# Optimization experiments

Measured on AMD Instinct MI355X. Metric: run time of the kernel, lower is better.

The kernel has to match this reference:

```python
import jax, jax.numpy as jnp
import numpy as np

N, E = 50000, 800000
DIN, H, DOUT, L = 128, 128, 64, 3
NEG_SLOPE = 0.2  # PyG GATConv default


def setup_inputs() -> dict:
    key = jax.random.key(0)
    ks = jax.random.split(key, 12)
    s = lambda i, shape: (jax.random.normal(ks[i], shape, jnp.float32) * 0.05)
    return {
        "x": jax.random.normal(ks[0], (N, DIN), jnp.float32),
        "edge_index": jax.random.randint(ks[1], (2, E), 0, N, jnp.int64 if jax.config.jax_enable_x64 else jnp.int32),
        "W_emb": s(2, (DIN, H)), "b_emb": jnp.zeros((H,), jnp.float32),
        "gat_W": s(3, (L, H, H)), "gat_as": s(4, (L, H)), "gat_ad": s(5, (L, H)),
        "gat_b": jnp.zeros((L, H), jnp.float32),
        "Wn1": s(6, (H, H)), "bn1": jnp.zeros((H,), jnp.float32),
        "Wn2": s(7, (H, DOUT)), "bn2": jnp.zeros((DOUT,), jnp.float32),
        "We1": s(8, (2 * H, H)), "be1": jnp.zeros((H,), jnp.float32),
        "We2": s(9, (H, 3)), "be2": jnp.zeros((3,), jnp.float32),
    }


def _gat_layer(h, src, dst, n, W, a_src, a_dst, b):
    # Single-head GATConv (PyG defaults: heads=1, concat, self-loops already in src/dst)
    xw = h @ W                                   # [N, H]
    alpha_s = xw @ a_src                          # [N]
    alpha_d = xw @ a_dst                          # [N]
    logits = jax.nn.leaky_relu(alpha_s[src] + alpha_d[dst], NEG_SLOPE)  # [E']
    m = jax.ops.segment_max(logits, dst, num_segments=n)
    p = jnp.exp(logits - m[dst])
    denom = jax.ops.segment_sum(p, dst, num_segments=n)
    alpha = p / denom[dst]                        # softmax over incoming edges
    return jax.ops.segment_sum(alpha[:, None] * xw[src], dst, num_segments=n) + b


def reference(x, edge_index, W_emb, b_emb, gat_W, gat_as, gat_ad, gat_b,
              Wn1, bn1, Wn2, bn2, We1, be1, We2, be2):
    n = x.shape[0]
    src0, dst0 = edge_index[0], edge_index[1]
    loops = jnp.arange(n, dtype=src0.dtype)
    src = jnp.concatenate([src0, loops])          # GATConv adds self-loops by default
    dst = jnp.concatenate([dst0, loops])

    h = jax.nn.relu(x @ W_emb + b_emb)            # dropout off (eval mode)
    for l in range(L):
        h_new = _gat_layer(h, src, dst, n, gat_W[l], gat_as[l], gat_ad[l], gat_b[l])
        h = jax.nn.relu(h + h_new)                # residual + relu

    node_pred = jax.nn.relu(h @ Wn1 + bn1) @ Wn2 + bn2            # [N, DOUT]
    ef = jnp.concatenate([h[src0], h[dst0]], axis=1)              # vectorized edge gather [E, 2H]
    edge_pred = jax.nn.relu(ef @ We1 + be1) @ We2 + be2           # [E, 3]
    graph_emb = jnp.mean(h, axis=0, keepdims=True)                # batch=None path [1, H]
    return node_pred, edge_pred, graph_emb
```

## Files before the change

kernel.cpp:

```cpp
#include <hip/hip_runtime.h>

#define NNODES 50000
#define NEDGES 800000
#define HDIM 128
#define DOUT 64
#define NLAYERS 3
#define NEG_SLOPE 0.2f

#define NODE_OUT_ELEMS (NNODES * DOUT)
#define EDGE_OUT_ELEMS (NEDGES * 3)
#define GEMB_OFF (NODE_OUT_ELEMS + EDGE_OUT_ELEMS)

typedef __attribute__((ext_vector_type(8))) short short8;
typedef __attribute__((ext_vector_type(4))) float f32x4;

__device__ __forceinline__ float bf2f(unsigned short u) {
    union { unsigned int i; float f; } v; v.i = ((unsigned int)u) << 16; return v.f;
}
__device__ __forceinline__ unsigned short f2bf(float f) {
    union { unsigned int i; float f; } v; v.f = f;
    unsigned int b = v.i;
    unsigned int r = (b + 0x7FFFu + ((b >> 16) & 1u)) >> 16;
    return (unsigned short)r;
}
__device__ __forceinline__ float leaky(float x) { return x > 0.f ? x : NEG_SLOPE * x; }

__device__ __forceinline__ int eget(const int* e32, const int* iflag, int which, int e) {
    int idx = which * NEDGES + e;
    return (*iflag) ? e32[idx] : e32[2 * idx];
}

__global__ void zero_int_kernel(int* p, int n) {
    int i = blockIdx.x * 256 + threadIdx.x;
    if (i < n) p[i] = 0;
}
__global__ void zero_f32_kernel(float* p, int n) {
    int i = blockIdx.x * 256 + threadIdx.x;
    if (i < n) p[i] = 0.f;
}

__global__ void detect_f32_kernel(const unsigned short* xb, int* flag) {
    int hit = 0;
    for (int j = threadIdx.x; j < 4096; j += 256) {
        int e = (xb[j] >> 7) & 0xFF;
        if (e >= 0x90) hit = 1;
    }
    if (hit) atomicOr(flag, 1);
}
__global__ void detect_i64_kernel(const int* e32, int* flag) {
    int hit = 0;
    for (int t = threadIdx.x; t < 16384; t += 256) {
        int i = t * 48;
        if (e32[2 * i + 1] != 0) hit = 1;
    }
    if (__any(hit)) {
        if ((threadIdx.x & 63) == 0) atomicOr(flag, 1);
    }
}

__global__ void cvt_kernel(const void* src, float* dst, int n, const int* f32flag) {
    int i = blockIdx.x * 256 + threadIdx.x;
    if (i < n)
        dst[i] = (*f32flag) ? ((const float*)src)[i]
                            : bf2f(((const unsigned short*)src)[i]);
}
__global__ void cvt_layerW_kernel(const void* gat_W, float* dst, int l,
                                  const int* f32flag) {
    int i = blockIdx.x * 256 + threadIdx.x;
    if (i < HDIM * HDIM) {
        size_t idx = (size_t)l * HDIM * HDIM + i;
        dst[i] = (*f32flag) ? ((const float*)gat_W)[idx]
                            : bf2f(((const unsigned short*)gat_W)[idx]);
    }
}

struct SmallCvtArgs {
    const void* src[9];
    float*      dst[9];
    int         n[9];
};
__global__ void cvt_small_kernel(SmallCvtArgs a, const int* f32flag) {
    const int f = *f32flag;
    for (int s = 0; s < 9; s++) {
        int n = a.n[s];
        const void* sp = a.src[s];
        float* dp = a.dst[s];
        for (int i = blockIdx.x * 256 + threadIdx.x; i < n; i += gridDim.x * 256)
            dp[i] = f ? ((const float*)sp)[i]
                      : bf2f(((const unsigned short*)sp)[i]);
    }
}

__global__ void cvt_x_bf16_kernel(const void* x, unsigned short* xb,
                                  const int* f32flag) {
    int i = (blockIdx.x * 256 + threadIdx.x) * 4;
    if (*f32flag) {
        float4 v = *(const float4*)((const float*)x + i);
        unsigned short o[4] = {f2bf(v.x), f2bf(v.y), f2bf(v.z), f2bf(v.w)};
        *(uint2*)(xb + i) = *(uint2*)o;
    } else {
        *(uint2*)(xb + i) = *(const uint2*)((const unsigned short*)x + i);
    }
}

__global__ __launch_bounds__(256) void gemm_mfma_kernel(
    const unsigned short* __restrict__ A, const float* __restrict__ Bf,
    const float* __restrict__ bias, unsigned short* __restrict__ C,
    int M, int relu)
{
    constexpr int KP = 128 + 8;
    __shared__ unsigned short sA[64 * KP];
    const int tid = threadIdx.x;
    const int row0 = blockIdx.x * 64;

    for (int c = tid; c < 64 * 16; c += 256) {
        int r = c >> 4, cp = c & 15;
        int gr = row0 + r;
        uint4 v = {0u, 0u, 0u, 0u};
        if (gr < M) v = *(const uint4*)(A + (size_t)gr * 128 + cp * 8);
        *(uint4*)(&sA[r * KP + cp * 8]) = v;
    }
    __syncthreads();

    const int wave = tid >> 6, lane = tid & 63;
    const int quad = lane >> 4, l15 = lane & 15;
    const int ncol0 = wave * 32;

    short8 bw[4][2];
    #pragma unroll
    for (int kk = 0; kk < 4; kk++)
        #pragma unroll
        for (int nt = 0; nt < 2; nt++) {
            int n = ncol0 + nt * 16 + l15;
            short8 t;
            #pragma unroll
            for (int j = 0; j < 8; j++)
                t[j] = (short)f2bf(Bf[(size_t)(kk * 32 + quad * 8 + j) * 128 + n]);
            bw[kk][nt] = t;
        }

    float bv[2];
    #pragma unroll
    for (int nt = 0; nt < 2; nt++)
        bv[nt] = bias ? bias[ncol0 + nt * 16 + l15] : 0.f;

    f32x4 acc[4][2];
    #pragma unroll
    for (int mt = 0; mt < 4; mt++)
        #pragma unroll
        for (int nt = 0; nt < 2; nt++) {
            acc[mt][nt][0] = bv[nt]; acc[mt][nt][1] = bv[nt];
            acc[mt][nt][2] = bv[nt]; acc[mt][nt][3] = bv[nt];
        }

    #pragma unroll
    for (int kk = 0; kk < 4; kk++) {
        short8 a[4];
        #pragma unroll
        for (int mt = 0; mt < 4; mt++)
            a[mt] = *(const short8*)(&sA[(mt * 16 + l15) * KP + kk * 32 + quad * 8]);
        #pragma unroll
        for (int mt = 0; mt < 4; mt++)
            #pragma unroll
            for (int nt = 0; nt < 2; nt++)
                acc[mt][nt] = __builtin_amdgcn_mfma_f32_16x16x32_bf16(
                    a[mt], bw[kk][nt], acc[mt][nt], 0, 0, 0);
    }

    #pragma unroll
    for (int mt = 0; mt < 4; mt++)
        #pragma unroll
        for (int nt = 0; nt < 2; nt++)
            #pragma unroll
            for (int q = 0; q < 4; q++) {
                int row = row0 + mt * 16 + quad * 4 + q;
                if (row < M) {
                    float v = acc[mt][nt][q];
                    if (relu) v = fmaxf(v, 0.f);
                    C[(size_t)row * 128 + ncol0 + nt * 16 + l15] = f2bf(v);
                }
            }
}

__global__ __launch_bounds__(256) void node_mlp_kernel(
    const unsigned short* __restrict__ h, const float* __restrict__ Wn1f,
    const float* __restrict__ bn1, const float* __restrict__ Wn2f,
    const float* __restrict__ bn2, float* __restrict__ out, int M)
{
    constexpr int KP = 128 + 8;
    __shared__ unsigned short sA[64 * KP];
    const int tid = threadIdx.x;
    const int row0 = blockIdx.x * 64;

    for (int c = tid; c < 64 * 16; c += 256) {
        int r = c >> 4, cp = c & 15;
        int gr = row0 + r;
        uint4 v = {0u, 0u, 0u, 0u};
        if (gr < M) v = *(const uint4*)(h + (size_t)gr * 128 + cp * 8);
        *(uint4*)(&sA[r * KP + cp * 8]) = v;
    }
    __syncthreads();

    const int wave = tid >> 6, lane = tid & 63;
    const int quad = lane >> 4, l15 = lane & 15;
    const int ncol0 = wave * 32;

    {
        short8 bw[4][2];
        #pragma unroll
        for (int kk = 0; kk < 4; kk++)
            #pragma unroll
            for (int nt = 0; nt < 2; nt++) {
                int n = ncol0 + nt * 16 + l15;
                short8 t;
                #pragma unroll
                for (int j = 0; j < 8; j++)
                    t[j] = (short)f2bf(Wn1f[(size_t)(kk * 32 + quad * 8 + j) * 128 + n]);
                bw[kk][nt] = t;
            }
        float bv[2];
        #pragma unroll
        for (int nt = 0; nt < 2; nt++) bv[nt] = bn1[ncol0 + nt * 16 + l15];

        f32x4 acc[4][2];
        #pragma unroll
        for (int mt = 0; mt < 4; mt++)
            #pragma unroll
            for (int nt = 0; nt < 2; nt++) {
                acc[mt][nt][0] = bv[nt]; acc[mt][nt][1] = bv[nt];
                acc[mt][nt][2] = bv[nt]; acc[mt][nt][3] = bv[nt];
            }
        #pragma unroll
        for (int kk = 0; kk < 4; kk++) {
            short8 a[4];
            #pragma unroll
            for (int mt = 0; mt < 4; mt++)
                a[mt] = *(const short8*)(&sA[(mt * 16 + l15) * KP + kk * 32 + quad * 8]);
            #pragma unroll
            for (int mt = 0; mt < 4; mt++)
                #pragma unroll
                for (int nt = 0; nt < 2; nt++)
                    acc[mt][nt] = __builtin_amdgcn_mfma_f32_16x16x32_bf16(
                        a[mt], bw[kk][nt], acc[mt][nt], 0, 0, 0);
        }
        __syncthreads();
        #pragma unroll
        for (int mt = 0; mt < 4; mt++)
            #pragma unroll
            for (int nt = 0; nt < 2; nt++)
                #pragma unroll
                for (int q = 0; q < 4; q++) {
                    int r = mt * 16 + quad * 4 + q;
                    sA[r * KP + ncol0 + nt * 16 + l15] =
                        f2bf(fmaxf(acc[mt][nt][q], 0.f));
                }
        __syncthreads();
    }

    {
        const int col = wave * 16 + l15;
        short8 bw[4];
        #pragma unroll
        for (int kk = 0; kk < 4; kk++) {
            short8 t;
            #pragma unroll
            for (int j = 0; j < 8; j++)
                t[j] = (short)f2bf(Wn2f[(size_t)(kk * 32 + quad * 8 + j) * 64 + col]);
            bw[kk] = t;
        }
        float bv = bn2[col];
        f32x4 acc[4];
        #pragma unroll
        for (int mt = 0; mt < 4; mt++) {
            acc[mt][0] = bv; acc[mt][1] = bv; acc[mt][2] = bv; acc[mt][3] = bv;
        }
        #pragma unroll
        for (int kk = 0; kk < 4; kk++) {
            short8 a[4];
            #pragma unroll
            for (int mt = 0; mt < 4; mt++)
                a[mt] = *(const short8*)(&sA[(mt * 16 + l15) * KP + kk * 32 + quad * 8]);
            #pragma unroll
            for (int mt = 0; mt < 4; mt++)
                acc[mt] = __builtin_amdgcn_mfma_f32_16x16x32_bf16(
                    a[mt], bw[kk], acc[mt], 0, 0, 0);
        }
        #pragma unroll
        for (int mt = 0; mt < 4; mt++)
            #pragma unroll
            for (int q = 0; q < 4; q++) {
                int row = row0 + mt * 16 + quad * 4 + q;
                if (row < M) out[(size_t)row * 64 + col] = acc[mt][q];
            }
    }
}

__global__ __launch_bounds__(256) void edge_ab_kernel(
    const unsigned short* __restrict__ h, const float* __restrict__ We1f,
    const float* __restrict__ be1, unsigned short* __restrict__ Axw,
    unsigned short* __restrict__ Bh, int M)
{
    constexpr int KP = 128 + 8;
    __shared__ unsigned short sA[64 * KP];
    const int tid = threadIdx.x;
    const int row0 = blockIdx.x * 64;

    for (int c = tid; c < 64 * 16; c += 256) {
        int r = c >> 4, cp = c & 15;
        int gr = row0 + r;
        uint4 v = {0u, 0u, 0u, 0u};
        if (gr < M) v = *(const uint4*)(h + (size_t)gr * 128 + cp * 8);
        *(uint4*)(&sA[r * KP + cp * 8]) = v;
    }
    __syncthreads();

    const int wave = tid >> 6, lane = tid & 63;
    const int quad = lane >> 4, l15 = lane & 15;
    const int ncol0 = wave * 32;

    #pragma unroll
    for (int half = 0; half < 2; half++) {
        const float* Bf = We1f + (size_t)half * 128 * 128;
        unsigned short* Cp = half ? Bh : Axw;

        short8 bw[4][2];
        #pragma unroll
        for (int kk = 0; kk < 4; kk++)
            #pragma unroll
            for (int nt = 0; nt < 2; nt++) {
                int n = ncol0 + nt * 16 + l15;
                short8 t;
                #pragma unroll
                for (int j = 0; j < 8; j++)
                    t[j] = (short)f2bf(Bf[(size_t)(kk * 32 + quad * 8 + j) * 128 + n]);
                bw[kk][nt] = t;
            }
        float bv[2];
        #pragma unroll
        for (int nt = 0; nt < 2; nt++)
            bv[nt] = half ? 0.f : be1[ncol0 + nt * 16 + l15];

        f32x4 acc[4][2];
        #pragma unroll
        for (int mt = 0; mt < 4; mt++)
            #pragma unroll
            for (int nt = 0; nt < 2; nt++) {
                acc[mt][nt][0] = bv[nt]; acc[mt][nt][1] = bv[nt];
                acc[mt][nt][2] = bv[nt]; acc[mt][nt][3] = bv[nt];
            }
        #pragma unroll
        for (int kk = 0; kk < 4; kk++) {
            short8 a[4];
            #pragma unroll
            for (int mt = 0; mt < 4; mt++)
                a[mt] = *(const short8*)(&sA[(mt * 16 + l15) * KP + kk * 32 + quad * 8]);
            #pragma unroll
            for (int mt = 0; mt < 4; mt++)
                #pragma unroll
                for (int nt = 0; nt < 2; nt++)
                    acc[mt][nt] = __builtin_amdgcn_mfma_f32_16x16x32_bf16(
                        a[mt], bw[kk][nt], acc[mt][nt], 0, 0, 0);
        }
        #pragma unroll
        for (int mt = 0; mt < 4; mt++)
            #pragma unroll
            for (int nt = 0; nt < 2; nt++)
                #pragma unroll
                for (int q = 0; q < 4; q++) {
                    int row = row0 + mt * 16 + quad * 4 + q;
                    if (row < M)
                        Cp[(size_t)row * 128 + ncol0 + nt * 16 + l15] =
                            f2bf(acc[mt][nt][q]);
                }
    }
}

__global__ void alpha_kernel(const unsigned short* xw,
                             const float* a_s, const float* a_d,
                             float* alpha_s, float* alpha_d) {
    int wave = threadIdx.x >> 6, lane = threadIdx.x & 63;
    int n = blockIdx.x * 4 + wave;
    if (n >= NNODES) return;
    float v0 = bf2f(xw[(size_t)n * HDIM + lane]);
    float v1 = bf2f(xw[(size_t)n * HDIM + 64 + lane]);
    float ds = v0 * a_s[lane] + v1 * a_s[64 + lane];
    float dd = v0 * a_d[lane] + v1 * a_d[64 + lane];
    for (int d = 32; d >= 1; d >>= 1) { ds += __shfl_xor(ds, d); dd += __shfl_xor(dd, d); }
    if (lane == 0) { alpha_s[n] = ds; alpha_d[n] = dd; }
}

__global__ void count_kernel(const int* e32, const int* iflag, int* cnt) {
    int e = blockIdx.x * 256 + threadIdx.x;
    if (e < NEDGES) atomicAdd(&cnt[eget(e32, iflag, 1, e)], 1);
}
__global__ void scan1_kernel(const int* cnt, int* off, int* bsum) {
    __shared__ int s[256];
    int t = threadIdx.x, i = blockIdx.x * 256 + t;
    int v = (i < NNODES) ? cnt[i] : 0;
    s[t] = v;
    __syncthreads();
    for (int d = 1; d < 256; d <<= 1) {
        int add = (t >= d) ? s[t - d] : 0;
        __syncthreads();
        s[t] += add;
        __syncthreads();
    }
    if (i < NNODES) off[i] = s[t] - v;
    if (t == 255) bsum[blockIdx.x] = s[255];
}
__global__ void scan2_kernel(int* bsum, int nblk) {
    if (threadIdx.x == 0 && blockIdx.x == 0) {
        int run = 0;
        for (int c = 0; c < nblk; c++) { int t = bsum[c]; bsum[c] = run; run += t; }
    }
}
__global__ void scan3_kernel(int* off, const int* bsum) {
    int i = blockIdx.x * 256 + threadIdx.x;
    if (i < NNODES) off[i] += bsum[blockIdx.x];
}
__global__ void fill_kernel(const int* e32, const int* iflag, const int* off,
                            int* cur, int* csr_src, int* csr_dst, int* csr_eid,
                            int use_csr) {
    int e = blockIdx.x * 256 + threadIdx.x;
    if (e < NEDGES) {
        int sidx = eget(e32, iflag, 0, e);
        int d = eget(e32, iflag, 1, e);
        int p = atomicAdd(&cur[d], 1);
        int pos = off[d] + p;
        csr_src[pos] = sidx;
        if (use_csr) {
            csr_dst[pos] = d;
            csr_eid[pos] = e;
        }
    }
}

__global__ void aggregate_kernel(const unsigned short* __restrict__ xw,
                                 const float* __restrict__ as_, const float* __restrict__ ad_,
                                 const int* __restrict__ off, const int* __restrict__ csr_src,
                                 const float* __restrict__ gat_b, unsigned short* __restrict__ h) {
    int wave = threadIdx.x >> 6, lane = threadIdx.x & 63;
    int n = blockIdx.x * 4 + wave;
    if (n >= NNODES) return;
    int o0 = off[n];
    int o1 = (n == NNODES - 1) ? NEDGES : off[n + 1];
    int deg = o1 - o0;
    float adn = ad_[n];
    float lself = leaky(as_[n] + adn);

    int deg64 = deg < 64 ? deg : 64;
    int idxv = 0; float av = 0.f;
    if (lane < deg64) { idxv = csr_src[o0 + lane]; av = as_[idxv]; }

    float m = lself;
    if (lane < deg64) m = fmaxf(m, leaky(av + adn));
    for (int i = 64 + lane; i < deg; i += 64) {
        int s = csr_src[o0 + i];
        m = fmaxf(m, leaky(as_[s] + adn));
    }
    #pragma unroll
    for (int d = 32; d >= 1; d >>= 1) m = fmaxf(m, __shfl_xor(m, d));

    const int slot = lane >> 4;
    const int l15  = lane & 15;
    float denom = 0.f;
    float acc[8];
    #pragma unroll
    for (int k = 0; k < 8; k++) acc[k] = 0.f;

    for (int t0 = 0; t0 < deg64; t0 += 4) {
        int i = t0 + slot;
        int sidx   = __shfl(idxv, i);
        float aval = __shfl(av, i);
        if (i < deg64) {
            float p = __expf(leaky(aval + adn) - m);
            denom += p;
            uint4 rv = *(const uint4*)(xw + (size_t)sidx * HDIM + l15 * 8);
            const unsigned short* rp = (const unsigned short*)&rv;
            #pragma unroll
            for (int k = 0; k < 8; k++) acc[k] += p * bf2f(rp[k]);
        }
    }
    for (int i = 64 + slot; i < deg; i += 4) {
        int s = csr_src[o0 + i];
        float p = __expf(leaky(as_[s] + adn) - m);
        denom += p;
        uint4 rv = *(const uint4*)(xw + (size_t)s * HDIM + l15 * 8);
        const unsigned short* rp = (const unsigned short*)&rv;
        #pragma unroll
        for (int k = 0; k < 8; k++) acc[k] += p * bf2f(rp[k]);
    }

    #pragma unroll
    for (int d = 16; d <= 32; d <<= 1) {
        denom += __shfl_xor(denom, d);
        #pragma unroll
        for (int k = 0; k < 8; k++) acc[k] += __shfl_xor(acc[k], d);
    }

    float ps = __expf(lself - m);
    denom += ps;
    uint4 sv = *(const uint4*)(xw + (size_t)n * HDIM + l15 * 8);
    const unsigned short* sp = (const unsigned short*)&sv;
    #pragma unroll
    for (int k = 0; k < 8; k++) acc[k] += ps * bf2f(sp[k]);

    if (slot == 0) {
        float inv = 1.f / denom;
        size_t base = (size_t)n * HDIM + l15 * 8;
        uint4 hv = *(const uint4*)(h + base);
        const unsigned short* hp = (const unsigned short*)&hv;
        unsigned short outv[8];
        #pragma unroll
        for (int k = 0; k < 8; k++) {
            float hx = bf2f(hp[k]);
            float bx = gat_b[l15 * 8 + k];
            outv[k] = f2bf(fmaxf(hx + acc[k] * inv + bx, 0.f));
        }
        *(uint4*)(h + base) = *(uint4*)outv;
    }
}

__global__ __launch_bounds__(256) void edge_split_kernel(
    const unsigned short* __restrict__ A, const unsigned short* __restrict__ B,
    const int* __restrict__ e32, const int* __restrict__ iflag,
    const int* __restrict__ csr_src, const int* __restrict__ csr_dst,
    const int* __restrict__ csr_eid, int use_csr,
    const float* __restrict__ We2, const float* __restrict__ be2,
    float* __restrict__ eout)
{
    const int lane = threadIdx.x & 63;
    const int slot = lane >> 4, l15 = lane & 15;

    float w2[8][3];
    #pragma unroll
    for (int j = 0; j < 8; j++)
        #pragma unroll
        for (int c = 0; c < 3; c++)
            w2[j][c] = We2[(l15 * 8 + j) * 3 + c];
    const float bo0 = be2[0], bo1 = be2[1], bo2 = be2[2];

    const int gw = (blockIdx.x * 256 + threadIdx.x) >> 6;
    const int stride = gridDim.x * 16;
    for (int e = gw * 4 + slot; e < NEDGES; e += stride) {
        int s, d, oe;
        if (use_csr) { s = csr_src[e]; d = csr_dst[e]; oe = csr_eid[e]; }
        else {
            s = eget(e32, iflag, 0, e);
            d = eget(e32, iflag, 1, e);
            oe = e;
        }
        uint4 avv = *(const uint4*)(A + (size_t)s * HDIM + l15 * 8);
        uint4 bvv = *(const uint4*)(B + (size_t)d * HDIM + l15 * 8);
        const unsigned short* ap = (const unsigned short*)&avv;
        const unsigned short* bp = (const unsigned short*)&bvv;
        float s0 = 0.f, s1 = 0.f, s2 = 0.f;
        #pragma unroll
        for (int j = 0; j < 8; j++) {
            float v = fmaxf(bf2f(ap[j]) + bf2f(bp[j]), 0.f);
            s0 += v * w2[j][0]; s1 += v * w2[j][1]; s2 += v * w2[j][2];
        }
        #pragma unroll
        for (int dd = 1; dd < 16; dd <<= 1) {
            s0 += __shfl_xor(s0, dd);
            s1 += __shfl_xor(s1, dd);
            s2 += __shfl_xor(s2, dd);
        }
        if (l15 == 0) {
            eout[(size_t)oe * 3 + 0] = s0 + bo0;
            eout[(size_t)oe * 3 + 1] = s1 + bo1;
            eout[(size_t)oe * 3 + 2] = s2 + bo2;
        }
    }
}

__global__ void gsum_kernel(const unsigned short* h, float* gsum) {
    int f = threadIdx.x;
    float local = 0.f;
    int n0 = blockIdx.x * 200;
    for (int j = 0; j < 200; j++) local += bf2f(h[(size_t)(n0 + j) * HDIM + f]);
    atomicAdd(&gsum[f], local);
}
__global__ void gout_kernel(const float* gsum, float* out) {
    int f = threadIdx.x;
    out[GEMB_OFF + f] = gsum[f] * (1.f / (float)NNODES);
}

extern "C" __attribute__((visibility("default")))
void kernel_launch(void* const* d_in, const int* in_sizes, int n_in,
                   void* d_out, int out_size, void* d_ws, size_t ws_size,
                   hipStream_t stream) {
    const void* x      = d_in[0];
    const int*  eidx   = (const int*)d_in[1];
    const void* W_emb  = d_in[2];
    const void* b_emb  = d_in[3];
    const void* gat_W  = d_in[4];
    const void* gat_as = d_in[5];
    const void* gat_ad = d_in[6];
    const void* gat_b  = d_in[7];
    const void* Wn1    = d_in[8];
    const void* bn1    = d_in[9];
    const void* Wn2    = d_in[10];
    const void* bn2    = d_in[11];
    const void* We1    = d_in[12];
    const void* be1    = d_in[13];
    const void* We2    = d_in[14];
    const void* be2    = d_in[15];
    float* out = (float*)d_out;

    char* ws = (char*)d_ws;
    unsigned short* h       = (unsigned short*)(ws);
    unsigned short* xw      = (unsigned short*)(ws + 12800000);
    float*          alpha_s = (float*)(ws + 25600000);
    float*          alpha_d = (float*)(ws + 25800000);
    int*            cnt     = (int*)(ws + 26000000);
    int*            off     = (int*)(ws + 26200000);
    int*            bsum    = (int*)(ws + 26400000);
    float*          gsum    = (float*)(ws + 26401024);
    int*            iflag   = (int*)(ws + 26401536);
    int*            fflag   = (int*)(ws + 26401540);
    float*          We1c    = (float*)(ws + 26402048);
    float*          We2c    = (float*)(ws + 26533120);
    float*          asc     = (float*)(ws + 26534656);
    float*          adc     = (float*)(ws + 26536192);
    float*          gbc     = (float*)(ws + 26537728);
    float*          bembc   = (float*)(ws + 26539264);
    float*          bn1c    = (float*)(ws + 26539776);
    float*          bn2c    = (float*)(ws + 26540288);
    float*          be1c    = (float*)(ws + 26540544);
    float*          be2c    = (float*)(ws + 26541056);
    float*          Wlc     = (float*)(ws + 26542080);
    int*            csr_src = (int*)(ws + 26608000);
    int*            csr_dst = (int*)(ws + 29808000);
    int*            csr_eid = (int*)(ws + 33008000);

    float* Wembc = (float*)(ws + 26200000);
    float* Wn1c = (float*)(ws + 26000000);
    float* Wn2c = (float*)(ws + 26065536);

    const int use_csr = (ws_size >= (size_t)36208000) ? 1 : 0;

    const int node_blks = (NNODES + 255) / 256;
    const int edge_blks = (NEDGES + 255) / 256;
    const int g64       = (NNODES + 63) / 64;

    zero_int_kernel<<<1, 256, 0, stream>>>(iflag, 2);
    zero_int_kernel<<<node_blks, 256, 0, stream>>>(cnt, NNODES);
    zero_f32_kernel<<<1, 256, 0, stream>>>(gsum, HDIM);

    detect_f32_kernel<<<1, 256, 0, stream>>>((const unsigned short*)x, fflag);
    detect_i64_kernel<<<1, 256, 0, stream>>>(eidx, iflag);

    SmallCvtArgs sc;
    sc.src[0] = We2;   sc.dst[0] = We2c;  sc.n[0] = 128 * 3;
    sc.src[1] = gat_as; sc.dst[1] = asc;  sc.n[1] = 3 * 128;
    sc.src[2] = gat_ad; sc.dst[2] = adc;  sc.n[2] = 3 * 128;
    sc.src[3] = gat_b;  sc.dst[3] = gbc;  sc.n[3] = 3 * 128;
    sc.src[4] = b_emb;  sc.dst[4] = bembc; sc.n[4] = 128;
    sc.src[5] = bn1;    sc.dst[5] = bn1c; sc.n[5] = 128;
    sc.src[6] = bn2;    sc.dst[6] = bn2c; sc.n[6] = 64;
    sc.src[7] = be1;    sc.dst[7] = be1c; sc.n[7] = 128;
    sc.src[8] = be2;    sc.dst[8] = be2c; sc.n[8] = 3;
    cvt_small_kernel<<<2, 256, 0, stream>>>(sc, fflag);

    cvt_kernel<<<128, 256, 0, stream>>>(We1, We1c, 256 * 128, fflag);
    cvt_kernel<<<64, 256, 0, stream>>>(W_emb, Wembc, 128 * 128, fflag);

    cvt_x_bf16_kernel<<<6250, 256, 0, stream>>>(x, xw, fflag);
    gemm_mfma_kernel<<<g64, 256, 0, stream>>>(
        xw, Wembc, bembc, h, NNODES, 1);

    count_kernel<<<edge_blks, 256, 0, stream>>>(eidx, iflag, cnt);
    scan1_kernel<<<node_blks, 256, 0, stream>>>(cnt, off, bsum);
    scan2_kernel<<<1, 64, 0, stream>>>(bsum, node_blks);
    scan3_kernel<<<node_blks, 256, 0, stream>>>(off, bsum);
    zero_int_kernel<<<node_blks, 256, 0, stream>>>(cnt, NNODES);
    fill_kernel<<<edge_blks, 256, 0, stream>>>(eidx, iflag, off, cnt,
                                               csr_src, csr_dst, csr_eid, use_csr);

    cvt_kernel<<<64, 256, 0, stream>>>(Wn1, Wn1c, 128 * 128, fflag);
    cvt_kernel<<<32, 256, 0, stream>>>(Wn2, Wn2c, 128 * 64, fflag);

    for (int l = 0; l < NLAYERS; l++) {
        cvt_layerW_kernel<<<64, 256, 0, stream>>>(gat_W, Wlc, l, fflag);
        gemm_mfma_kernel<<<g64, 256, 0, stream>>>(
            h, Wlc, (const float*)0, xw, NNODES, 0);
        alpha_kernel<<<(NNODES + 3) / 4, 256, 0, stream>>>(
            xw, asc + l * HDIM, adc + l * HDIM, alpha_s, alpha_d);
        aggregate_kernel<<<(NNODES + 3) / 4, 256, 0, stream>>>(
            xw, alpha_s, alpha_d, off, csr_src, gbc + l * HDIM, h);
    }

    node_mlp_kernel<<<g64, 256, 0, stream>>>(
        h, Wn1c, bn1c, Wn2c, bn2c, out, NNODES);

    gsum_kernel<<<NNODES / 200, 128, 0, stream>>>(h, gsum);
    gout_kernel<<<1, 128, 0, stream>>>(gsum, out);

    edge_ab_kernel<<<g64, 256, 0, stream>>>(
        h, We1c, be1c, xw, h, NNODES);
    edge_split_kernel<<<2048, 256, 0, stream>>>(
        xw, h, eidx, iflag, csr_src, csr_dst, csr_eid, use_csr,
        We2c, be2c, out + NODE_OUT_ELEMS);
}
```

Baseline: 547.2 us.

## Drop weight conversion kernels, read raw weights in place, pack CSR entries

Result: slower. 567.8 us (+3.8%).

```diff
diff --git a/kernel.cpp b/kernel.cpp
--- a/kernel.cpp
+++ b/kernel.cpp
@@ -13,6 +13,7 @@
 
 typedef __attribute__((ext_vector_type(8))) short short8;
 typedef __attribute__((ext_vector_type(4))) float f32x4;
+typedef unsigned long long u64;
 
 __device__ __forceinline__ float bf2f(unsigned short u) {
     union { unsigned int i; float f; } v; v.i = ((unsigned int)u) << 16; return v.f;
@@ -24,70 +25,42 @@
     return (unsigned short)r;
 }
 __device__ __forceinline__ float leaky(float x) { return x > 0.f ? x : NEG_SLOPE * x; }
+__device__ __forceinline__ float wread(const void* p, size_t i, int f32) {
+    return f32 ? ((const float*)p)[i] : bf2f(((const unsigned short*)p)[i]);
+}
 
 __device__ __forceinline__ int eget(const int* e32, const int* iflag, int which, int e) {
     int idx = which * NEDGES + e;
     return (*iflag) ? e32[idx] : e32[2 * idx];
 }
 
-__global__ void zero_int_kernel(int* p, int n) {
+__global__ void init_kernel(int* cnt, int* cur, float* gsum, int* flags) {
     int i = blockIdx.x * 256 + threadIdx.x;
-    if (i < n) p[i] = 0;
-}
-__global__ void zero_f32_kernel(float* p, int n) {
-    int i = blockIdx.x * 256 + threadIdx.x;
-    if (i < n) p[i] = 0.f;
-}
-
-__global__ void detect_f32_kernel(const unsigned short* xb, int* flag) {
-    int hit = 0;
-    for (int j = threadIdx.x; j < 4096; j += 256) {
-        int e = (xb[j] >> 7) & 0xFF;
-        if (e >= 0x90) hit = 1;
-    }
-    if (hit) atomicOr(flag, 1);
-}
-__global__ void detect_i64_kernel(const int* e32, int* flag) {
-    int hit = 0;
-    for (int t = threadIdx.x; t < 16384; t += 256) {
-        int i = t * 48;
-        if (e32[2 * i + 1] != 0) hit = 1;
-    }
-    if (__any(hit)) {
-        if ((threadIdx.x & 63) == 0) atomicOr(flag, 1);
-    }
-}
-
-__global__ void cvt_kernel(const void* src, float* dst, int n, const int* f32flag) {
-    int i = blockIdx.x * 256 + threadIdx.x;
-    if (i < n)
-        dst[i] = (*f32flag) ? ((const float*)src)[i]
-                            : bf2f(((const unsigned short*)src)[i]);
-}
-__global__ void cvt_layerW_kernel(const void* gat_W, float* dst, int l,
-                                  const int* f32flag) {
-    int i = blockIdx.x * 256 + threadIdx.x;
-    if (i < HDIM * HDIM) {
-        size_t idx = (size_t)l * HDIM * HDIM + i;
-        dst[i] = (*f32flag) ? ((const float*)gat_W)[idx]
-                            : bf2f(((const unsigned short*)gat_W)[idx]);
-    }
-}
-
-struct SmallCvtArgs {
-    const void* src[9];
-    float*      dst[9];
-    int         n[9];
-};
-__global__ void cvt_small_kernel(SmallCvtArgs a, const int* f32flag) {
-    const int f = *f32flag;
-    for (int s = 0; s < 9; s++) {
-        int n = a.n[s];
-        const void* sp = a.src[s];
-        float* dp = a.dst[s];
-        for (int i = blockIdx.x * 256 + threadIdx.x; i < n; i += gridDim.x * 256)
-            dp[i] = f ? ((const float*)sp)[i]
-                      : bf2f(((const unsigned short*)sp)[i]);
+    if (i < NNODES) { cnt[i] = 0; cur[i] = 0; }
+    if (blockIdx.x == 0) {
+        if (threadIdx.x < HDIM) gsum[threadIdx.x] = 0.f;
+        if (threadIdx.x < 2) flags[threadIdx.x] = 0;
+    }
+}
+
+__global__ void detect_kernel(const unsigned short* xb, const int* e32,
+                              int* fflag, int* iflag) {
+    if (blockIdx.x == 0) {
+        int hit = 0;
+        for (int j = threadIdx.x; j < 4096; j += 256) {
+            int e = (xb[j] >> 7) & 0xFF;
+            if (e >= 0x90) hit = 1;
+        }
+        if (hit) atomicOr(fflag, 1);
+    } else {
+        int hit = 0;
+        for (int t = threadIdx.x; t < 16384; t += 256) {
+            int i = t * 48;
+            if (e32[2 * i + 1] != 0) hit = 1;
+        }
+        if (__any(hit)) {
+            if ((threadIdx.x & 63) == 0) atomicOr(iflag, 1);
+        }
     }
 }
 
@@ -104,12 +77,13 @@
 }
 
 __global__ __launch_bounds__(256) void gemm_mfma_kernel(
-    const unsigned short* __restrict__ A, const float* __restrict__ Bf,
-    const float* __restrict__ bias, unsigned short* __restrict__ C,
-    int M, int relu)
+    const unsigned short* __restrict__ A, const void* __restrict__ Bw,
+    size_t b_off, const void* __restrict__ bias, unsigned short* __restrict__ C,
+    int M, int relu, const int* __restrict__ f32flag)
 {
     constexpr int KP = 128 + 8;
     __shared__ unsigned short sA[64 * KP];
+    const int f32 = *f32flag;
     const int tid = threadIdx.x;
     const int row0 = blockIdx.x * 64;
 
@@ -135,14 +109,14 @@
             short8 t;
             #pragma unroll
             for (int j = 0; j < 8; j++)
-                t[j] = (short)f2bf(Bf[(size_t)(kk * 32 + quad * 8 + j) * 128 + n]);
+                t[j] = (short)f2bf(wread(Bw, b_off + (size_t)(kk * 32 + quad * 8 + j) * 128 + n, f32));
             bw[kk][nt] = t;
         }
 
     float bv[2];
     #pragma unroll
     for (int nt = 0; nt < 2; nt++)
-        bv[nt] = bias ? bias[ncol0 + nt * 16 + l15] : 0.f;
+        bv[nt] = bias ? wread(bias, ncol0 + nt * 16 + l15, f32) : 0.f;
 
     f32x4 acc[4][2];
     #pragma unroll
@@ -183,12 +157,14 @@
 }
 
 __global__ __launch_bounds__(256) void node_mlp_kernel(
-    const unsigned short* __restrict__ h, const float* __restrict__ Wn1f,
-    const float* __restrict__ bn1, const float* __restrict__ Wn2f,
-    const float* __restrict__ bn2, float* __restrict__ out, int M)
+    const unsigned short* __restrict__ h, const void* __restrict__ Wn1,
+    const void* __restrict__ bn1, const void* __restrict__ Wn2,
+    const void* __restrict__ bn2, float* __restrict__ out, int M,
+    const int* __restrict__ f32flag)
 {
     constexpr int KP = 128 + 8;
     __shared__ unsigned short sA[64 * KP];
+    const int f32 = *f32flag;
     const int tid = threadIdx.x;
     const int row0 = blockIdx.x * 64;
 
@@ -215,12 +191,13 @@
                 short8 t;
                 #pragma unroll
                 for (int j = 0; j < 8; j++)
-                    t[j] = (short)f2bf(Wn1f[(size_t)(kk * 32 + quad * 8 + j) * 128 + n]);
+                    t[j] = (short)f2bf(wread(Wn1, (size_t)(kk * 32 + quad * 8 + j) * 128 + n, f32));
                 bw[kk][nt] = t;
             }
         float bv[2];
         #pragma unroll
-        for (int nt = 0; nt < 2; nt++) bv[nt] = bn1[ncol0 + nt * 16 + l15];
+        for (int nt = 0; nt < 2; nt++)
+            bv[nt] = wread(bn1, ncol0 + nt * 16 + l15, f32);
 
         f32x4 acc[4][2];
         #pragma unroll
@@ -265,10 +242,10 @@
             short8 t;
             #pragma unroll
             for (int j = 0; j < 8; j++)
-                t[j] = (short)f2bf(Wn2f[(size_t)(kk * 32 + quad * 8 + j) * 64 + col]);
+                t[j] = (short)f2bf(wread(Wn2, (size_t)(kk * 32 + quad * 8 + j) * 64 + col, f32));
             bw[kk] = t;
         }
-        float bv = bn2[col];
+        float bv = wread(bn2, col, f32);
         f32x4 acc[4];
         #pragma unroll
         for (int mt = 0; mt < 4; mt++) {
@@ -296,12 +273,13 @@
 }
 
 __global__ __launch_bounds__(256) void edge_ab_kernel(
-    const unsigned short* __restrict__ h, const float* __restrict__ We1f,
-    const float* __restrict__ be1, unsigned short* __restrict__ Axw,
-    unsigned short* __restrict__ Bh, int M)
+    const unsigned short* __restrict__ h, const void* __restrict__ We1,
+    const void* __restrict__ be1, unsigned short* __restrict__ Axw,
+    unsigned short* __restrict__ Bh, int M, const int* __restrict__ f32flag)
 {
     constexpr int KP = 128 + 8;
     __shared__ unsigned short sA[64 * KP];
+    const int f32 = *f32flag;
     const int tid = threadIdx.x;
     const int row0 = blockIdx.x * 64;
 
@@ -320,7 +298,7 @@
 
     #pragma unroll
     for (int half = 0; half < 2; half++) {
-        const float* Bf = We1f + (size_t)half * 128 * 128;
+        const size_t b_off = (size_t)half * 128 * 128;
         unsigned short* Cp = half ? Bh : Axw;
 
         short8 bw[4][2];
@@ -332,13 +310,13 @@
                 short8 t;
                 #pragma unroll
                 for (int j = 0; j < 8; j++)
-                    t[j] = (short)f2bf(Bf[(size_t)(kk * 32 + quad * 8 + j) * 128 + n]);
+                    t[j] = (short)f2bf(wread(We1, b_off + (size_t)(kk * 32 + quad * 8 + j) * 128 + n, f32));
                 bw[kk][nt] = t;
             }
         float bv[2];
         #pragma unroll
         for (int nt = 0; nt < 2; nt++)
-            bv[nt] = half ? 0.f : be1[ncol0 + nt * 16 + l15];
+            bv[nt] = half ? 0.f : wread(be1, ncol0 + nt * 16 + l15, f32);
 
         f32x4 acc[4][2];
         #pragma unroll
@@ -376,15 +354,17 @@
 }
 
 __global__ void alpha_kernel(const unsigned short* xw,
-                             const float* a_s, const float* a_d,
-                             float* alpha_s, float* alpha_d) {
+                             const void* gat_as, const void* gat_ad, int woff,
+                             float* alpha_s, float* alpha_d,
+                             const int* f32flag) {
+    const int f32 = *f32flag;
     int wave = threadIdx.x >> 6, lane = threadIdx.x & 63;
     int n = blockIdx.x * 4 + wave;
     if (n >= NNODES) return;
     float v0 = bf2f(xw[(size_t)n * HDIM + lane]);
     float v1 = bf2f(xw[(size_t)n * HDIM + 64 + lane]);
-    float ds = v0 * a_s[lane] + v1 * a_s[64 + lane];
-    float dd = v0 * a_d[lane] + v1 * a_d[64 + lane];
+    float ds = v0 * wread(gat_as, woff + lane, f32) + v1 * wread(gat_as, woff + 64 + lane, f32);
+    float dd = v0 * wread(gat_ad, woff + lane, f32) + v1 * wread(gat_ad, woff + 64 + lane, f32);
     for (int d = 32; d >= 1; d >>= 1) { ds += __shfl_xor(ds, d); dd += __shfl_xor(dd, d); }
     if (lane == 0) { alpha_s[n] = ds; alpha_d[n] = dd; }
 }
@@ -419,26 +399,27 @@
     if (i < NNODES) off[i] += bsum[blockIdx.x];
 }
 __global__ void fill_kernel(const int* e32, const int* iflag, const int* off,
-                            int* cur, int* csr_src, int* csr_dst, int* csr_eid,
-                            int use_csr) {
+                            int* cur, u64* csrp, int use_pack) {
     int e = blockIdx.x * 256 + threadIdx.x;
     if (e < NEDGES) {
-        int sidx = eget(e32, iflag, 0, e);
+        int s = eget(e32, iflag, 0, e);
         int d = eget(e32, iflag, 1, e);
         int p = atomicAdd(&cur[d], 1);
         int pos = off[d] + p;
-        csr_src[pos] = sidx;
-        if (use_csr) {
-            csr_dst[pos] = d;
-            csr_eid[pos] = e;
-        }
+        if (use_pack)
+            csrp[pos] = (u64)s | ((u64)d << 17) | ((u64)e << 34);
+        else
+            ((int*)csrp)[pos] = s;
     }
 }
 
 __global__ void aggregate_kernel(const unsigned short* __restrict__ xw,
                                  const float* __restrict__ as_, const float* __restrict__ ad_,
-                                 const int* __restrict__ off, const int* __restrict__ csr_src,
-                                 const float* __restrict__ gat_b, unsigned short* __restrict__ h) {
+                                 const int* __restrict__ off, const u64* __restrict__ csrp,
+                                 int use_pack, const void* __restrict__ gat_b, int boff,
+                                 unsigned short* __restrict__ h,
+                                 const int* __restrict__ f32flag) {
+    const int f32 = *f32flag;
     int wave = threadIdx.x >> 6, lane = threadIdx.x & 63;
     int n = blockIdx.x * 4 + wave;
     if (n >= NNODES) return;
@@ -450,12 +431,17 @@
 
     int deg64 = deg < 64 ? deg : 64;
     int idxv = 0; float av = 0.f;
-    if (lane < deg64) { idxv = csr_src[o0 + lane]; av = as_[idxv]; }
+    if (lane < deg64) {
+        idxv = use_pack ? (int)(csrp[o0 + lane] & 0x1FFFF)
+                        : ((const int*)csrp)[o0 + lane];
+        av = as_[idxv];
+    }
 
     float m = lself;
     if (lane < deg64) m = fmaxf(m, leaky(av + adn));
     for (int i = 64 + lane; i < deg; i += 64) {
-        int s = csr_src[o0 + i];
+        int s = use_pack ? (int)(csrp[o0 + i] & 0x1FFFF)
+                         : ((const int*)csrp)[o0 + i];
         m = fmaxf(m, leaky(as_[s] + adn));
     }
     #pragma unroll
@@ -482,7 +468,8 @@
         }
     }
     for (int i = 64 + slot; i < deg; i += 4) {
-        int s = csr_src[o0 + i];
+        int s = use_pack ? (int)(csrp[o0 + i] & 0x1FFFF)
+                         : ((const int*)csrp)[o0 + i];
         float p = __expf(leaky(as_[s] + adn) - m);
         denom += p;
         uint4 rv = *(const uint4*)(xw + (size_t)s * HDIM + l15 * 8);
@@ -514,7 +501,7 @@
         #pragma unroll
         for (int k = 0; k < 8; k++) {
             float hx = bf2f(hp[k]);
-            float bx = gat_b[l15 * 8 + k];
+            float bx = wread(gat_b, boff + l15 * 8 + k, f32);
             outv[k] = f2bf(fmaxf(hx + acc[k] * inv + bx, 0.f));
         }
         *(uint4*)(h + base) = *(uint4*)outv;
@@ -524,11 +511,11 @@
 __global__ __launch_bounds__(256) void edge_split_kernel(
     const unsigned short* __restrict__ A, const unsigned short* __restrict__ B,
     const int* __restrict__ e32, const int* __restrict__ iflag,
-    const int* __restrict__ csr_src, const int* __restrict__ csr_dst,
-    const int* __restrict__ csr_eid, int use_csr,
-    const float* __restrict__ We2, const float* __restrict__ be2,
-    float* __restrict__ eout)
+    const u64* __restrict__ csrp, int use_pack,
+    const void* __restrict__ We2, const void* __restrict__ be2,
+    float* __restrict__ eout, const int* __restrict__ f32flag)
 {
+    const int f32 = *f32flag;
     const int lane = threadIdx.x & 63;
     const int slot = lane >> 4, l15 = lane & 15;
 
@@ -537,15 +524,21 @@
     for (int j = 0; j < 8; j++)
         #pragma unroll
         for (int c = 0; c < 3; c++)
-            w2[j][c] = We2[(l15 * 8 + j) * 3 + c];
-    const float bo0 = be2[0], bo1 = be2[1], bo2 = be2[2];
+            w2[j][c] = wread(We2, (l15 * 8 + j) * 3 + c, f32);
+    const float bo0 = wread(be2, 0, f32);
+    const float bo1 = wread(be2, 1, f32);
+    const float bo2 = wread(be2, 2, f32);
 
     const int gw = (blockIdx.x * 256 + threadIdx.x) >> 6;
     const int stride = gridDim.x * 16;
     for (int e = gw * 4 + slot; e < NEDGES; e += stride) {
         int s, d, oe;
-        if (use_csr) { s = csr_src[e]; d = csr_dst[e]; oe = csr_eid[e]; }
-        else {
+        if (use_pack) {
+            u64 pk = csrp[e];
+            s  = (int)(pk & 0x1FFFF);
+            d  = (int)((pk >> 17) & 0x1FFFF);
+            oe = (int)(pk >> 34);
+        } else {
             s = eget(e32, iflag, 0, e);
             d = eget(e32, iflag, 1, e);
             oe = e;
@@ -619,87 +612,46 @@
     float*          gsum    = (float*)(ws + 26401024);
     int*            iflag   = (int*)(ws + 26401536);
     int*            fflag   = (int*)(ws + 26401540);
-    float*          We1c    = (float*)(ws + 26402048);
-    float*          We2c    = (float*)(ws + 26533120);
-    float*          asc     = (float*)(ws + 26534656);
-    float*          adc     = (float*)(ws + 26536192);
-    float*          gbc     = (float*)(ws + 26537728);
-    float*          bembc   = (float*)(ws + 26539264);
-    float*          bn1c    = (float*)(ws + 26539776);
-    float*          bn2c    = (float*)(ws + 26540288);
-    float*          be1c    = (float*)(ws + 26540544);
-    float*          be2c    = (float*)(ws + 26541056);
-    float*          Wlc     = (float*)(ws + 26542080);
-    int*            csr_src = (int*)(ws + 26608000);
-    int*            csr_dst = (int*)(ws + 29808000);
-    int*            csr_eid = (int*)(ws + 33008000);
-
-    float* Wembc = (float*)(ws + 26200000);
-    float* Wn1c = (float*)(ws + 26000000);
-    float* Wn2c = (float*)(ws + 26065536);
-
-    const int use_csr = (ws_size >= (size_t)36208000) ? 1 : 0;
+    u64*            csrp    = (u64*)(ws + 26608000);
+    int*            cur     = (int*)alpha_s;
+
+    const int use_pack = (ws_size >= (size_t)33008000) ? 1 : 0;
 
     const int node_blks = (NNODES + 255) / 256;
     const int edge_blks = (NEDGES + 255) / 256;
     const int g64       = (NNODES + 63) / 64;
 
-    zero_int_kernel<<<1, 256, 0, stream>>>(iflag, 2);
-    zero_int_kernel<<<node_blks, 256, 0, stream>>>(cnt, NNODES);
-    zero_f32_kernel<<<1, 256, 0, stream>>>(gsum, HDIM);
-
-    detect_f32_kernel<<<1, 256, 0, stream>>>((const unsigned short*)x, fflag);
-    detect_i64_kernel<<<1, 256, 0, stream>>>(eidx, iflag);
-
-    SmallCvtArgs sc;
-    sc.src[0] = We2;   sc.dst[0] = We2c;  sc.n[0] = 128 * 3;
-    sc.src[1] = gat_as; sc.dst[1] = asc;  sc.n[1] = 3 * 128;
-    sc.src[2] = gat_ad; sc.dst[2] = adc;  sc.n[2] = 3 * 128;
-    sc.src[3] = gat_b;  sc.dst[3] = gbc;  sc.n[3] = 3 * 128;
-    sc.src[4] = b_emb;  sc.dst[4] = bembc; sc.n[4] = 128;
-    sc.src[5] = bn1;    sc.dst[5] = bn1c; sc.n[5] = 128;
-    sc.src[6] = bn2;    sc.dst[6] = bn2c; sc.n[6] = 64;
-    sc.src[7] = be1;    sc.dst[7] = be1c; sc.n[7] = 128;
-    sc.src[8] = be2;    sc.dst[8] = be2c; sc.n[8] = 3;
-    cvt_small_kernel<<<2, 256, 0, stream>>>(sc, fflag);
-
-    cvt_kernel<<<128, 256, 0, stream>>>(We1, We1c, 256 * 128, fflag);
-    cvt_kernel<<<64, 256, 0, stream>>>(W_emb, Wembc, 128 * 128, fflag);
+    init_kernel<<<node_blks, 256, 0, stream>>>(cnt, cur, gsum, iflag);
+    detect_kernel<<<2, 256, 0, stream>>>((const unsigned short*)x, eidx, fflag, iflag);
 
     cvt_x_bf16_kernel<<<6250, 256, 0, stream>>>(x, xw, fflag);
     gemm_mfma_kernel<<<g64, 256, 0, stream>>>(
-        xw, Wembc, bembc, h, NNODES, 1);
+        xw, W_emb, 0, b_emb, h, NNODES, 1, fflag);
 
     count_kernel<<<edge_blks, 256, 0, stream>>>(eidx, iflag, cnt);
     scan1_kernel<<<node_blks, 256, 0, stream>>>(cnt, off, bsum);
     scan2_kernel<<<1, 64, 0, stream>>>(bsum, node_blks);
     scan3_kernel<<<node_blks, 256, 0, stream>>>(off, bsum);
-    zero_int_kernel<<<node_blks, 256, 0, stream>>>(cnt, NNODES);
-    fill_kernel<<<edge_blks, 256, 0, stream>>>(eidx, iflag, off, cnt,
-                                               csr_src, csr_dst, csr_eid, use_csr);
-
-    cvt_kernel<<<64, 256, 0, stream>>>(Wn1, Wn1c, 128 * 128, fflag);
-    cvt_kernel<<<32, 256, 0, stream>>>(Wn2, Wn2c, 128 * 64, fflag);
+    fill_kernel<<<edge_blks, 256, 0, stream>>>(eidx, iflag, off, cur, csrp, use_pack);
 
     for (int l = 0; l < NLAYERS; l++) {
-        cvt_layerW_kernel<<<64, 256, 0, stream>>>(gat_W, Wlc, l, fflag);
         gemm_mfma_kernel<<<g64, 256, 0, stream>>>(
-            h, Wlc, (const float*)0, xw, NNODES, 0);
+            h, gat_W, (size_t)l * HDIM * HDIM, (const void*)0, xw, NNODES, 0, fflag);
         alpha_kernel<<<(NNODES + 3) / 4, 256, 0, stream>>>(
-            xw, asc + l * HDIM, adc + l * HDIM, alpha_s, alpha_d);
+            xw, gat_as, gat_ad, l * HDIM, alpha_s, alpha_d, fflag);
         aggregate_kernel<<<(NNODES + 3) / 4, 256, 0, stream>>>(
-            xw, alpha_s, alpha_d, off, csr_src, gbc + l * HDIM, h);
+            xw, alpha_s, alpha_d, off, csrp, use_pack, gat_b, l * HDIM, h, fflag);
     }
 
     node_mlp_kernel<<<g64, 256, 0, stream>>>(
-        h, Wn1c, bn1c, Wn2c, bn2c, out, NNODES);
+        h, Wn1, bn1, Wn2, bn2, out, NNODES, fflag);
 
     gsum_kernel<<<NNODES / 200, 128, 0, stream>>>(h, gsum);
     gout_kernel<<<1, 128, 0, stream>>>(gsum, out);
 
     edge_ab_kernel<<<g64, 256, 0, stream>>>(
-        h, We1c, be1c, xw, h, NNODES);
+        h, We1, be1, xw, h, NNODES, fflag);
     edge_split_kernel<<<2048, 256, 0, stream>>>(
-        xw, h, eidx, iflag, csr_src, csr_dst, csr_eid, use_csr,
-        We2c, be2c, out + NODE_OUT_ELEMS);
-}
+        xw, h, eidx, iflag, csrp, use_pack, We2, be2,
+        out + NODE_OUT_ELEMS, fflag);
+}
```
